# Optimization experiments

Hardware: AMD Instinct MI355X
Metric: run time of the kernel (lower is better)

## Reference

```python
import jax, jax.numpy as jnp
import numpy as np
from jax import lax

# physiological constants from the source module
DT = 1.0
TAU_L = 10.0
G_B = 0.6
G_L = 1.0 / TAU_L
LAMBDA_MAX = 0.35
STEPS = int(50 / DT)

IN_SIZE, HID, OUT, BATCH = 1024, 2048, 512, 4096


def setup_inputs() -> dict:
    key = jax.random.key(0)
    k1, k2, k3, k4, k5, k6 = jax.random.split(key, 6)
    psp = jax.random.uniform(k1, (IN_SIZE, BATCH), dtype=jnp.float32)  # |mm(spikes,kernel)| is >=0
    label = jax.random.uniform(k2, (BATCH, OUT), dtype=jnp.float32)    # teaching current I
    # Linear params init: uniform(-0.1, 0.1) as in the torch module
    W_h = jax.random.uniform(k3, (HID, IN_SIZE), minval=-0.1, maxval=0.1, dtype=jnp.float32)
    b_h = jax.random.uniform(k4, (HID,), minval=-0.1, maxval=0.1, dtype=jnp.float32)
    W_o = jax.random.uniform(k5, (OUT, HID), minval=-0.1, maxval=0.1, dtype=jnp.float32)
    b_o = jax.random.uniform(k6, (OUT,), minval=-0.1, maxval=0.1, dtype=jnp.float32)
    return {"psp": psp, "label": label, "W_h": W_h, "b_h": b_h, "W_o": W_o, "b_o": b_o}


def reference(psp, label, W_h, b_h, W_o, b_o):
    a = DT / TAU_L
    gr = G_B / G_L  # = 6.0
    x = psp.T  # [B, in] -- Hidden_layer transposes basal_input
    # psp is constant over the time loop, so the hidden basal GEMM hoists out
    basal_V_h = x @ W_h.T + b_h  # [B, HID]
    soma_h0 = jnp.zeros_like(basal_V_h)
    soma_o0 = jnp.zeros((x.shape[0], W_o.shape[0]), dtype=x.dtype)

    def step(carry, _):
        soma_h, soma_o = carry
        # hidden two-compartment leaky integration
        soma_h = soma_h + a * (-soma_h + gr * (basal_V_h - soma_h))
        rate_h = LAMBDA_MAX * jax.nn.sigmoid(soma_h)  # [B, HID]
        basal_V_o = rate_h @ W_o.T + b_o              # [B, OUT]
        # output layer, training (test=False) branch: nudged by teaching current I=label
        soma_o = soma_o + a * (-soma_o + gr * (basal_V_o - soma_o) + label - soma_o)
        return (soma_h, soma_o), None

    (soma_h, soma_o), _ = lax.scan(step, (soma_h0, soma_o0), None, length=STEPS)
    return LAMBDA_MAX * jax.nn.sigmoid(soma_o)  # out_layer.spike_rate, [B, OUT]
```

## Files before the change

kernel.cpp:

```cpp
#include <hip/hip_runtime.h>
#include <hip/hip_bf16.h>


typedef __bf16 bf16_t;
typedef __bf16 bf16x8 __attribute__((ext_vector_type(8)));
typedef __bf16 bf16x4v __attribute__((ext_vector_type(4)));
typedef float f32x4 __attribute__((ext_vector_type(4)));
typedef float f32x16 __attribute__((ext_vector_type(16)));
typedef int i32x4 __attribute__((ext_vector_type(4)));
typedef int i32x8 __attribute__((ext_vector_type(8)));

#define GLD_TO_LDS16(gp, lp)                                            \
  __builtin_amdgcn_global_load_lds(                                     \
      (__attribute__((address_space(1))) void*)(void*)(gp),             \
      (__attribute__((address_space(3))) void*)(lp), 16, 0, 0)

__device__ inline int pk4_fp8(float x, float y, float z, float w) {
  int lo = __builtin_amdgcn_cvt_pk_fp8_f32(x, y, 0, false);
  return __builtin_amdgcn_cvt_pk_fp8_f32(z, w, lo, true);
}

__global__ __launch_bounds__(256) void prep(
    const float* __restrict__ psp, unsigned char* __restrict__ pspT8,
    const float4* __restrict__ wh, int* __restrict__ wh8,
    const float4* __restrict__ wo, bf16x4v* __restrict__ wob) {
  __shared__ float tile[64][65];
  const int tid = threadIdx.x;
  const int b = blockIdx.x;
  const int c0 = (b & 63) * 64;
  const int r0 = (b >> 6) * 64;
  const int tx = tid & 63;
  const int ty = tid >> 6;
#pragma unroll
  for (int i = 0; i < 16; ++i) {
    const int r = ty + i * 4;
    tile[r][tx] = psp[(size_t)(r0 + r) * 4096 + c0 + tx];
  }
  {
    const int i1 = b * 512 + tid;
#pragma unroll
    for (int u = 0; u < 2; ++u) {
      const int idx = i1 + u * 256;
      const float4 v = wh[idx];
      wh8[idx] = pk4_fp8(v.x, v.y, v.z, v.w);
    }
  }
  {
    const int i2 = b * 256 + tid;
    const float4 v = wo[i2];
    bf16x4v o;
    o.x = (bf16_t)v.x; o.y = (bf16_t)v.y; o.z = (bf16_t)v.z; o.w = (bf16_t)v.w;
    wob[i2] = o;
  }
  __syncthreads();
  const int brow0 = tid >> 4;
  const int c4 = (tid & 15) * 4;
#pragma unroll
  for (int i = 0; i < 4; ++i) {
    const int brow = brow0 + i * 16;
    const int packed = pk4_fp8(tile[c4][brow], tile[c4 + 1][brow],
                               tile[c4 + 2][brow], tile[c4 + 3][brow]);
    *(int*)(pspT8 + (size_t)(c0 + brow) * 1024 + r0 + c4) = packed;
  }
}

__global__ __launch_bounds__(256, 2) void gemm1_nt(
    const unsigned char* __restrict__ A8, const unsigned char* __restrict__ B8,
    const float* __restrict__ bias, bf16_t* __restrict__ C,
    int M, int N, int K) {
  __shared__ __align__(16) unsigned char sA[2][128 * 128];
  __shared__ __align__(16) unsigned char sB[2][128 * 128];

  const int tid = threadIdx.x;
  const int wave = tid >> 6;
  const int lane = tid & 63;
  const int bm = blockIdx.x * 128;
  const int bn = blockIdx.y * 128;
  const int wm = (wave & 1) * 64;
  const int wn = (wave >> 1) * 64;

  f32x16 acc[2][2] = {};

  const int srow8 = lane >> 3;
  const int gseg = (lane & 7) ^ srow8;
  const unsigned char* Ag =
      A8 + (size_t)(bm + wave * 32 + srow8) * 1024 + gseg * 16;
  const unsigned char* Bg =
      B8 + (size_t)(bn + wave * 32 + srow8) * 1024 + gseg * 16;
  const int dst = wave * 4096;

  const int col = lane & 31;
  const int g = lane >> 5;

  for (int t = 0; t < 4; ++t) {
    const int kb = t * 256;
#pragma unroll
    for (int h = 0; h < 2; ++h) {
#pragma unroll
      for (int c = 0; c < 4; ++c) {
        GLD_TO_LDS16(Ag + kb + h * 128 + (size_t)(c * 8) * 1024,
                     sA[h] + dst + c * 1024);
        GLD_TO_LDS16(Bg + kb + h * 128 + (size_t)(c * 8) * 1024,
                     sB[h] + dst + c * 1024);
      }
    }
    __syncthreads();

#pragma unroll
    for (int p = 0; p < 4; ++p) {
      const int h = p >> 1;
      const int s0 = (p & 1) * 4 + 2 * g;
      i32x8 av[2], bv[2];
#pragma unroll
      for (int i = 0; i < 2; ++i) {
        const int rr = wm + i * 32 + col;
        const unsigned char* base = sA[h] + rr * 128;
        const i32x4 lo = *(const i32x4*)(base + ((s0 ^ (rr & 7)) * 16));
        const i32x4 hi = *(const i32x4*)(base + (((s0 + 1) ^ (rr & 7)) * 16));
        av[i] = __builtin_shufflevector(lo, hi, 0, 1, 2, 3, 4, 5, 6, 7);
      }
#pragma unroll
      for (int j = 0; j < 2; ++j) {
        const int rr = wn + j * 32 + col;
        const unsigned char* base = sB[h] + rr * 128;
        const i32x4 lo = *(const i32x4*)(base + ((s0 ^ (rr & 7)) * 16));
        const i32x4 hi = *(const i32x4*)(base + (((s0 + 1) ^ (rr & 7)) * 16));
        bv[j] = __builtin_shufflevector(lo, hi, 0, 1, 2, 3, 4, 5, 6, 7);
      }
      __builtin_amdgcn_s_setprio(1);
#pragma unroll
      for (int i = 0; i < 2; ++i)
#pragma unroll
        for (int j = 0; j < 2; ++j)
          acc[i][j] = __builtin_amdgcn_mfma_scale_f32_32x32x64_f8f6f4(
              av[i], bv[j], acc[i][j], 0, 0,
              0, 0x7F7F7F7F, 0, 0x7F7F7F7F);
      __builtin_amdgcn_s_setprio(0);
    }
    __syncthreads();
  }

  const int rbase = 4 * g;
#pragma unroll
  for (int j = 0; j < 2; ++j) {
    const int gn = bn + wn + j * 32 + col;
    const float bj = bias[gn];
#pragma unroll
    for (int i = 0; i < 2; ++i) {
#pragma unroll
      for (int r = 0; r < 16; ++r) {
        const int gm = bm + wm + i * 32 + (r & 3) + 8 * (r >> 2) + rbase;
        const float z = 0.8571428571428571f * (acc[i][j][r] + bj);
        C[(size_t)gm * N + gn] = (bf16_t)(0.35f / (1.0f + __expf(-z)));
      }
    }
  }
}

__global__ __launch_bounds__(256, 2) void gemm2_nt(
    const bf16_t* __restrict__ A, const bf16_t* __restrict__ Bt,
    const float* __restrict__ bias, const float* __restrict__ lbl,
    float* __restrict__ out, int M, int N, int K) {
  __shared__ __align__(16) bf16_t sA[4][64 * 64];
  __shared__ __align__(16) bf16_t sB[4][64 * 64];

  const int tid = threadIdx.x;
  const int wave = tid >> 6;
  const int lane = tid & 63;
  const int bm = blockIdx.x * 64;
  const int bn = blockIdx.y * 64;
  const int wm = (wave & 1) * 32;
  const int wn = (wave >> 1) * 32;

  f32x4 acc[2][2] = {};

  const int srow8 = lane >> 3;
  const int gseg = (lane & 7) ^ srow8;
  const bf16_t* Ag = A + (size_t)(bm + wave * 16 + srow8) * K + gseg * 8;
  const bf16_t* Bg = Bt + (size_t)(bn + wave * 16 + srow8) * K + gseg * 8;
  const int dst = wave * 1024;

  const int fr = lane & 15;
  const int qh = lane >> 4;
  const int NT = K / 256;

  for (int t = 0; t < NT; ++t) {
    const int k0 = t * 256;
#pragma unroll
    for (int p = 0; p < 4; ++p) {
#pragma unroll
      for (int c = 0; c < 2; ++c) {
        GLD_TO_LDS16(Ag + k0 + p * 64 + (size_t)(c * 8) * K,
                     sA[p] + dst + c * 512);
        GLD_TO_LDS16(Bg + k0 + p * 64 + (size_t)(c * 8) * K,
                     sB[p] + dst + c * 512);
      }
    }
    __syncthreads();

#pragma unroll
    for (int ks = 0; ks < 8; ++ks) {
      const int pnl = ks >> 1;
      const int q2 = (ks * 4 + qh) & 7;
      bf16x8 av[2], bv[2];
#pragma unroll
      for (int i = 0; i < 2; ++i) {
        const int ra = wm + i * 16 + fr;
        av[i] = *(const bf16x8*)(sA[pnl] + ra * 64 + ((q2 ^ (ra & 7)) * 8));
      }
#pragma unroll
      for (int j = 0; j < 2; ++j) {
        const int rb = wn + j * 16 + fr;
        bv[j] = *(const bf16x8*)(sB[pnl] + rb * 64 + ((q2 ^ (rb & 7)) * 8));
      }
#pragma unroll
      for (int i = 0; i < 2; ++i)
#pragma unroll
        for (int j = 0; j < 2; ++j)
          acc[i][j] = __builtin_amdgcn_mfma_f32_16x16x32_bf16(
              av[i], bv[j], acc[i][j], 0, 0, 0);
    }
    __syncthreads();
  }

  const int cm0 = qh * 4;
#pragma unroll
  for (int j = 0; j < 2; ++j) {
    const int gn = bn + wn + j * 16 + fr;
    const float bj = bias[gn];
#pragma unroll
    for (int i = 0; i < 2; ++i) {
#pragma unroll
      for (int r = 0; r < 4; ++r) {
        const int gm = bm + wm + i * 16 + cm0 + r;
        const float z =
            0.75f * (acc[i][j][r] + bj) + 0.125f * lbl[(size_t)gm * N + gn];
        out[(size_t)gm * N + gn] = 0.35f / (1.0f + __expf(-z));
      }
    }
  }
}

extern "C" void kernel_launch(void* const* d_in, const int* in_sizes, int n_in,
                              void* d_out, int out_size, void* d_ws, size_t ws_size,
                              hipStream_t stream) {
  constexpr int IN = 1024, HID = 2048, OUT = 512, B = 4096;
  const float* psp = (const float*)d_in[0];
  const float* lbl = (const float*)d_in[1];
  const float* W_h = (const float*)d_in[2];
  const float* b_h = (const float*)d_in[3];
  const float* W_o = (const float*)d_in[4];
  const float* b_o = (const float*)d_in[5];
  float* out = (float*)d_out;

  unsigned char* Whb8 = (unsigned char*)d_ws;
  bf16_t* Wob = (bf16_t*)(Whb8 + (size_t)HID * IN);
  unsigned char* pspT8 = (unsigned char*)(Wob + (size_t)OUT * HID);
  bf16_t* Rm = (bf16_t*)(pspT8 + (size_t)B * IN);

  prep<<<1024, 256, 0, stream>>>(
      psp, pspT8, (const float4*)W_h, (int*)Whb8, (const float4*)W_o,
      (bf16x4v*)Wob);
  gemm1_nt<<<dim3(B / 128, HID / 128), 256, 0, stream>>>(
      pspT8, Whb8, b_h, Rm, B, HID, IN);
  gemm2_nt<<<dim3(B / 64, OUT / 64), 256, 0, stream>>>(
      Rm, Wob, b_o, lbl, out, B, OUT, HID);
}
```

Baseline: 117.3 us.

## Quantize hidden rates and output weights to FP8 with hi/lo split in GEMM2

GEMM1 now writes the hidden sigmoid rates as centered FP8 (rate minus 0.175) instead of bf16, halving the intermediate's memory traffic. W_o is split into FP8 high and low residual parts, and GEMM2 uses two scaled 32x32x64 FP8 MFMAs per k-step in place of bf16 MFMAs. A per-row sum of W_o, computed in prep with a block reduction, restores the centering offset in the bias. This cuts bytes moved and raises MFMA throughput, at the cost of FP8 rounding error on the activations and extra prep work.

Measured after the change: 114.6 us. -2.3%, faster.

```diff
diff --git a/kernel.cpp b/kernel.cpp
--- a/kernel.cpp
+++ b/kernel.cpp
@@ -3,8 +3,6 @@
 
 
 typedef __bf16 bf16_t;
-typedef __bf16 bf16x8 __attribute__((ext_vector_type(8)));
-typedef __bf16 bf16x4v __attribute__((ext_vector_type(4)));
 typedef float f32x4 __attribute__((ext_vector_type(4)));
 typedef float f32x16 __attribute__((ext_vector_type(16)));
 typedef int i32x4 __attribute__((ext_vector_type(4)));
@@ -20,11 +18,23 @@
   return __builtin_amdgcn_cvt_pk_fp8_f32(z, w, lo, true);
 }
 
+__device__ inline unsigned char fp8_1(float x) {
+  return (unsigned char)(__builtin_amdgcn_cvt_pk_fp8_f32(x, x, 0, false) & 0xFF);
+}
+
+__device__ inline float dec_e4m3(int b) {
+  const int s = (b >> 7) & 1, e = (b >> 3) & 15, m = b & 7;
+  const float v = e ? ldexpf((float)(8 + m), e - 10) : ldexpf((float)m, -9);
+  return s ? -v : v;
+}
+
 __global__ __launch_bounds__(256) void prep(
     const float* __restrict__ psp, unsigned char* __restrict__ pspT8,
     const float4* __restrict__ wh, int* __restrict__ wh8,
-    const float4* __restrict__ wo, bf16x4v* __restrict__ wob) {
+    const float4* __restrict__ wo, int* __restrict__ wo8hi,
+    int* __restrict__ wo8lo, float* __restrict__ rs2) {
   __shared__ float tile[64][65];
+  __shared__ float red[256];
   const int tid = threadIdx.x;
   const int b = blockIdx.x;
   const int c0 = (b & 63) * 64;
@@ -45,14 +55,27 @@
       wh8[idx] = pk4_fp8(v.x, v.y, v.z, v.w);
     }
   }
+  float psum;
   {
     const int i2 = b * 256 + tid;
     const float4 v = wo[i2];
-    bf16x4v o;
-    o.x = (bf16_t)v.x; o.y = (bf16_t)v.y; o.z = (bf16_t)v.z; o.w = (bf16_t)v.w;
-    wob[i2] = o;
-  }
+    const int hi = pk4_fp8(v.x, v.y, v.z, v.w);
+    const float hx = dec_e4m3(hi & 0xFF), hy = dec_e4m3((hi >> 8) & 0xFF);
+    const float hz = dec_e4m3((hi >> 16) & 0xFF), hw = dec_e4m3((hi >> 24) & 0xFF);
+    const int lo = pk4_fp8(v.x - hx, v.y - hy, v.z - hz, v.w - hw);
+    wo8hi[i2] = hi;
+    wo8lo[i2] = lo;
+    psum = hx + hy + hz + hw + dec_e4m3(lo & 0xFF) + dec_e4m3((lo >> 8) & 0xFF) +
+           dec_e4m3((lo >> 16) & 0xFF) + dec_e4m3((lo >> 24) & 0xFF);
+  }
+  red[tid] = psum;
   __syncthreads();
+#pragma unroll
+  for (int s = 128; s > 0; s >>= 1) {
+    if (tid < s) red[tid] += red[tid + s];
+    __syncthreads();
+  }
+  if (tid == 0) rs2[b] = red[0];
   const int brow0 = tid >> 4;
   const int c4 = (tid & 15) * 4;
 #pragma unroll
@@ -66,7 +89,7 @@
 
 __global__ __launch_bounds__(256, 2) void gemm1_nt(
     const unsigned char* __restrict__ A8, const unsigned char* __restrict__ B8,
-    const float* __restrict__ bias, bf16_t* __restrict__ C,
+    const float* __restrict__ bias, unsigned char* __restrict__ C8,
     int M, int N, int K) {
   __shared__ __align__(16) unsigned char sA[2][128 * 128];
   __shared__ __align__(16) unsigned char sB[2][128 * 128];
@@ -151,18 +174,20 @@
       for (int r = 0; r < 16; ++r) {
         const int gm = bm + wm + i * 32 + (r & 3) + 8 * (r >> 2) + rbase;
         const float z = 0.8571428571428571f * (acc[i][j][r] + bj);
-        C[(size_t)gm * N + gn] = (bf16_t)(0.35f / (1.0f + __expf(-z)));
+        C8[(size_t)gm * N + gn] = fp8_1(0.35f / (1.0f + __expf(-z)) - 0.175f);
       }
     }
   }
 }
 
 __global__ __launch_bounds__(256, 2) void gemm2_nt(
-    const bf16_t* __restrict__ A, const bf16_t* __restrict__ Bt,
-    const float* __restrict__ bias, const float* __restrict__ lbl,
+    const unsigned char* __restrict__ A8, const unsigned char* __restrict__ Bh8,
+    const unsigned char* __restrict__ Bl8, const float* __restrict__ bias,
+    const float* __restrict__ rs2, const float* __restrict__ lbl,
     float* __restrict__ out, int M, int N, int K) {
-  __shared__ __align__(16) bf16_t sA[4][64 * 64];
-  __shared__ __align__(16) bf16_t sB[4][64 * 64];
+  __shared__ __align__(16) unsigned char sA[2][64 * 128];
+  __shared__ __align__(16) unsigned char sBh[2][64 * 128];
+  __shared__ __align__(16) unsigned char sBl[2][64 * 128];
 
   const int tid = threadIdx.x;
   const int wave = tid >> 6;
@@ -172,72 +197,78 @@
   const int wm = (wave & 1) * 32;
   const int wn = (wave >> 1) * 32;
 
-  f32x4 acc[2][2] = {};
+  f32x16 acc = {};
 
   const int srow8 = lane >> 3;
   const int gseg = (lane & 7) ^ srow8;
-  const bf16_t* Ag = A + (size_t)(bm + wave * 16 + srow8) * K + gseg * 8;
-  const bf16_t* Bg = Bt + (size_t)(bn + wave * 16 + srow8) * K + gseg * 8;
-  const int dst = wave * 1024;
-
-  const int fr = lane & 15;
-  const int qh = lane >> 4;
-  const int NT = K / 256;
-
-  for (int t = 0; t < NT; ++t) {
-    const int k0 = t * 256;
+  const unsigned char* Ag =
+      A8 + (size_t)(bm + wave * 16 + srow8) * 2048 + gseg * 16;
+  const unsigned char* Bhg =
+      Bh8 + (size_t)(bn + wave * 16 + srow8) * 2048 + gseg * 16;
+  const unsigned char* Blg =
+      Bl8 + (size_t)(bn + wave * 16 + srow8) * 2048 + gseg * 16;
+  const int dst = wave * 2048;
+
+  const int col = lane & 31;
+  const int g = lane >> 5;
+
+  for (int t = 0; t < 8; ++t) {
+    const int kb = t * 256;
+#pragma unroll
+    for (int h = 0; h < 2; ++h) {
+#pragma unroll
+      for (int c = 0; c < 2; ++c) {
+        GLD_TO_LDS16(Ag + kb + h * 128 + (size_t)(c * 8) * 2048,
+                     sA[h] + dst + c * 1024);
+        GLD_TO_LDS16(Bhg + kb + h * 128 + (size_t)(c * 8) * 2048,
+                     sBh[h] + dst + c * 1024);
+        GLD_TO_LDS16(Blg + kb + h * 128 + (size_t)(c * 8) * 2048,
+                     sBl[h] + dst + c * 1024);
+      }
+    }
+    __syncthreads();
+
 #pragma unroll
     for (int p = 0; p < 4; ++p) {
-#pragma unroll
-      for (int c = 0; c < 2; ++c) {
-        GLD_TO_LDS16(Ag + k0 + p * 64 + (size_t)(c * 8) * K,
-                     sA[p] + dst + c * 512);
-        GLD_TO_LDS16(Bg + k0 + p * 64 + (size_t)(c * 8) * K,
-                     sB[p] + dst + c * 512);
-      }
-    }
-    __syncthreads();
-
-#pragma unroll
-    for (int ks = 0; ks < 8; ++ks) {
-      const int pnl = ks >> 1;
-      const int q2 = (ks * 4 + qh) & 7;
-      bf16x8 av[2], bv[2];
-#pragma unroll
-      for (int i = 0; i < 2; ++i) {
-        const int ra = wm + i * 16 + fr;
-        av[i] = *(const bf16x8*)(sA[pnl] + ra * 64 + ((q2 ^ (ra & 7)) * 8));
-      }
-#pragma unroll
-      for (int j = 0; j < 2; ++j) {
-        const int rb = wn + j * 16 + fr;
-        bv[j] = *(const bf16x8*)(sB[pnl] + rb * 64 + ((q2 ^ (rb & 7)) * 8));
-      }
-#pragma unroll
-      for (int i = 0; i < 2; ++i)
-#pragma unroll
-        for (int j = 0; j < 2; ++j)
-          acc[i][j] = __builtin_amdgcn_mfma_f32_16x16x32_bf16(
-              av[i], bv[j], acc[i][j], 0, 0, 0);
-    }
-    __syncthreads();
-  }
-
-  const int cm0 = qh * 4;
-#pragma unroll
-  for (int j = 0; j < 2; ++j) {
-    const int gn = bn + wn + j * 16 + fr;
-    const float bj = bias[gn];
-#pragma unroll
-    for (int i = 0; i < 2; ++i) {
-#pragma unroll
-      for (int r = 0; r < 4; ++r) {
-        const int gm = bm + wm + i * 16 + cm0 + r;
-        const float z =
-            0.75f * (acc[i][j][r] + bj) + 0.125f * lbl[(size_t)gm * N + gn];
-        out[(size_t)gm * N + gn] = 0.35f / (1.0f + __expf(-z));
-      }
-    }
+      const int h = p >> 1;
+      const int s0 = (p & 1) * 4 + 2 * g;
+      i32x8 av, bhv, blv;
+      {
+        const int rr = wm + col;
+        const unsigned char* base = sA[h] + rr * 128;
+        const i32x4 lo = *(const i32x4*)(base + ((s0 ^ (rr & 7)) * 16));
+        const i32x4 hi = *(const i32x4*)(base + (((s0 + 1) ^ (rr & 7)) * 16));
+        av = __builtin_shufflevector(lo, hi, 0, 1, 2, 3, 4, 5, 6, 7);
+      }
+      {
+        const int rr = wn + col;
+        const unsigned char* bb = sBh[h] + rr * 128;
+        const i32x4 lo = *(const i32x4*)(bb + ((s0 ^ (rr & 7)) * 16));
+        const i32x4 hi = *(const i32x4*)(bb + (((s0 + 1) ^ (rr & 7)) * 16));
+        bhv = __builtin_shufflevector(lo, hi, 0, 1, 2, 3, 4, 5, 6, 7);
+        const unsigned char* bl = sBl[h] + rr * 128;
+        const i32x4 lo2 = *(const i32x4*)(bl + ((s0 ^ (rr & 7)) * 16));
+        const i32x4 hi2 = *(const i32x4*)(bl + (((s0 + 1) ^ (rr & 7)) * 16));
+        blv = __builtin_shufflevector(lo2, hi2, 0, 1, 2, 3, 4, 5, 6, 7);
+      }
+      __builtin_amdgcn_s_setprio(1);
+      acc = __builtin_amdgcn_mfma_scale_f32_32x32x64_f8f6f4(
+          av, bhv, acc, 0, 0, 0, 0x7F7F7F7F, 0, 0x7F7F7F7F);
+      acc = __builtin_amdgcn_mfma_scale_f32_32x32x64_f8f6f4(
+          av, blv, acc, 0, 0, 0, 0x7F7F7F7F, 0, 0x7F7F7F7F);
+      __builtin_amdgcn_s_setprio(0);
+    }
+    __syncthreads();
+  }
+
+  const int rbase = 4 * g;
+  const int gn = bn + wn + col;
+  const float bj = bias[gn] + 0.175f * (rs2[2 * gn] + rs2[2 * gn + 1]);
+#pragma unroll
+  for (int r = 0; r < 16; ++r) {
+    const int gm = bm + wm + (r & 3) + 8 * (r >> 2) + rbase;
+    const float z = 0.75f * (acc[r] + bj) + 0.125f * lbl[(size_t)gm * N + gn];
+    out[(size_t)gm * N + gn] = 0.35f / (1.0f + __expf(-z));
   }
 }
 
@@ -254,15 +285,17 @@
   float* out = (float*)d_out;
 
   unsigned char* Whb8 = (unsigned char*)d_ws;
-  bf16_t* Wob = (bf16_t*)(Whb8 + (size_t)HID * IN);
-  unsigned char* pspT8 = (unsigned char*)(Wob + (size_t)OUT * HID);
-  bf16_t* Rm = (bf16_t*)(pspT8 + (size_t)B * IN);
+  unsigned char* Wo8hi = Whb8 + (size_t)HID * IN;
+  unsigned char* Wo8lo = Wo8hi + (size_t)OUT * HID;
+  unsigned char* pspT8 = Wo8lo + (size_t)OUT * HID;
+  unsigned char* Dm8 = pspT8 + (size_t)B * IN;
+  float* rs2 = (float*)(Dm8 + (size_t)B * HID);
 
   prep<<<1024, 256, 0, stream>>>(
       psp, pspT8, (const float4*)W_h, (int*)Whb8, (const float4*)W_o,
-      (bf16x4v*)Wob);
+      (int*)Wo8hi, (int*)Wo8lo, rs2);
   gemm1_nt<<<dim3(B / 128, HID / 128), 256, 0, stream>>>(
-      pspT8, Whb8, b_h, Rm, B, HID, IN);
+      pspT8, Whb8, b_h, Dm8, B, HID, IN);
   gemm2_nt<<<dim3(B / 64, OUT / 64), 256, 0, stream>>>(
-      Rm, Wob, b_o, lbl, out, B, OUT, HID);
-}
+      Dm8, Wo8hi, Wo8lo, b_o, rs2, lbl, out, B, OUT, HID);
+}
```
